# Performance work log

Hardware: AMD Instinct MI355X
Metric: run time of the kernel (lower is better)

## Reference

```python
import jax, jax.numpy as jnp
import numpy as np
from jax import lax

HDIM = 64
KDIM = 256
RATE = 0.999
EPS = 1e-6


def _l2norm(v, axis=-1):
    # matches F.normalize(dim=1) with default eps=1e-12
    n = jnp.sqrt(jnp.sum(v * v, axis=axis, keepdims=True))
    return v / jnp.maximum(n, 1e-12)


def setup_inputs() -> dict:
    key = jax.random.key(0)
    k1, k2 = jax.random.split(key)
    x = jax.random.normal(k1, (4, HDIM, 256, 256), dtype=jnp.float32)
    units = jax.random.normal(k2, (KDIM, HDIM), dtype=jnp.float32)  # nn.Embedding(kdim, hdim)
    return {"x": x, "units": units}


def reference(x, units):
    b, c, h, w = x.shape
    xf = jnp.transpose(x, (0, 2, 3, 1)).reshape(-1, c)        # [n, c]
    xd = lax.stop_gradient(xf)                                 # update uses x.detach()
    m = lax.stop_gradient(units)                               # units.weight.data (no grad)

    xn = _l2norm(xf, axis=1)                                   # [n, c]
    mn = _l2norm(m, axis=1)                                    # [k, c]
    score = jnp.matmul(xn, mn.T)                               # [n, k]
    n = xf.shape[0]

    for _ in range(3):
        # EMA codebook update from hard assignments (scatter-sum via segment_sum)
        idx = jnp.argmax(score, axis=1)                        # [n]
        embed_sum = jax.ops.segment_sum(xd, idx, num_segments=KDIM)          # [k, c]
        counts = jax.ops.segment_sum(jnp.ones((n,), xd.dtype), idx, num_segments=KDIM)  # [k]
        embed_mean = embed_sum / (counts + EPS)[:, None]       # [k, c]
        m = m * RATE + embed_mean * (1.0 - RATE)
        mn = _l2norm(m, axis=1)
        score = jnp.matmul(xn, mn.T)

    soft_label = jax.nn.softmax(score, axis=1)                 # [n, k]
    out = jnp.matmul(soft_label, m)                            # [n, c]
    out = out.reshape(b, h, w, c).transpose(0, 3, 1, 2)        # [b, c, h, w]
    return out
```

## Files before the change

kernel.cpp:

```cpp
#include <hip/hip_runtime.h>
#include <math.h>

#define HW 65536
#define NROW 262144
#define KK 256
#define R3_F 0.997002999f
#define E3_F 0.002997001f
#define NPART 1024

typedef __attribute__((ext_vector_type(8))) short short8;
typedef __attribute__((ext_vector_type(4))) float floatx4;

#define MFMA16(A, B, C) __builtin_amdgcn_mfma_f32_16x16x32_bf16(A, B, C, 0, 0, 0)

union U8 { unsigned u[4]; short8 v; };

__device__ __forceinline__ unsigned short f2bf(float f) {
    unsigned u = __float_as_uint(f);
    u = (u + 0x7FFFu + ((u >> 16) & 1u)) >> 16;
    return (unsigned short)u;
}
__device__ __forceinline__ float bf2f(unsigned hi) {
    return __uint_as_float(hi << 16);
}

__global__ __launch_bounds__(64) void k_init(const float* __restrict__ units,
                                             float* __restrict__ m,
                                             unsigned short* __restrict__ mn) {
    int k = blockIdx.x, c = threadIdx.x;
    float v = units[(k << 6) | c];
    m[(k << 6) | c] = v;
    float ss = v * v;
#pragma unroll
    for (int off = 32; off; off >>= 1) ss += __shfl_xor(ss, off, 64);
    mn[(k << 6) | c] = f2bf(v / fmaxf(sqrtf(ss), 1e-12f));
}

__global__ __launch_bounds__(512, 4) void k_pass1(const float* __restrict__ x,
                                                  const unsigned short* __restrict__ mn,
                                                  unsigned short* __restrict__ psums,
                                                  float* __restrict__ pcnts,
                                                  float* __restrict__ inv_norms,
                                                  unsigned short* __restrict__ xn,
                                                  int write_xn) {
    __shared__ unsigned short xrc[256 * 74];
    __shared__ unsigned short smn[KK * 72];
    __shared__ unsigned int lidx[64];
    __shared__ float lcnt[256];
    __shared__ float sInv[256];
    unsigned int* xrc32 = (unsigned int*)xrc;

    const int tid = threadIdx.x, wave = tid >> 6, lane = tid & 63;
    const int quad = lane >> 4, l15 = lane & 15;
    const int rowbase = blockIdx.x * 256;
    const int b = rowbase >> 16, p0 = rowbase & 65535;
    const float* xb = x + (((size_t)(b * 64)) << 16) + p0;

    if (tid < 256) lcnt[tid] = 0.f;
    for (int i = tid; i < KK * 64; i += 512) smn[(i >> 6) * 72 + (i & 63)] = mn[i];

    {
        int cp = tid >> 4, rq = tid & 15;
        const float* xc0 = xb + (((size_t)(cp * 2)) << 16);
        const float* xc1 = xb + (((size_t)(cp * 2 + 1)) << 16);
#pragma unroll
        for (int i = 0; i < 4; i++) {
            int rg = rq + i * 16;
            float4 v0 = *(const float4*)(xc0 + rg * 4);
            float4 v1 = *(const float4*)(xc1 + rg * 4);
            xrc32[(rg * 4 + 0) * 37 + cp] = (unsigned)f2bf(v0.x) | ((unsigned)f2bf(v1.x) << 16);
            xrc32[(rg * 4 + 1) * 37 + cp] = (unsigned)f2bf(v0.y) | ((unsigned)f2bf(v1.y) << 16);
            xrc32[(rg * 4 + 2) * 37 + cp] = (unsigned)f2bf(v0.z) | ((unsigned)f2bf(v1.z) << 16);
            xrc32[(rg * 4 + 3) * 37 + cp] = (unsigned)f2bf(v0.w) | ((unsigned)f2bf(v1.w) << 16);
        }
    }
    __syncthreads();

    if (tid < 256) {
        float ss = 0.f;
#pragma unroll
        for (int i = 0; i < 32; i++) {
            unsigned u = xrc32[tid * 37 + i];
            float f0 = bf2f(u & 0xffffu), f1 = bf2f(u >> 16);
            ss += f0 * f0 + f1 * f1;
        }
        float invv = 1.0f / fmaxf(sqrtf(ss), 1e-12f);
        sInv[tid] = invv;
        inv_norms[rowbase + tid] = invv;
    }
    __syncthreads();

#pragma unroll
    for (int mt = 0; mt < 2; mt++) {
        int rloc = wave * 32 + mt * 16 + l15;
        U8 a0, a1;
#pragma unroll
        for (int i = 0; i < 4; i++) {
            a0.u[i] = xrc32[rloc * 37 + quad * 4 + i];
            a1.u[i] = xrc32[rloc * 37 + 16 + quad * 4 + i];
        }
        int best[4] = {0, 0, 0, 0};
        for (int nt = 0; nt < 16; nt++) {
            const unsigned short* bp = &smn[(nt * 16 + l15) * 72 + quad * 8];
            short8 b0 = *(const short8*)bp;
            short8 b1 = *(const short8*)(bp + 32);
            floatx4 acc = {0.f, 0.f, 0.f, 0.f};
            acc = MFMA16(a0.v, b0, acc);
            acc = MFMA16(a1.v, b1, acc);
#pragma unroll
            for (int rg = 0; rg < 4; rg++) {
                int pk = (__float_as_int(acc[rg] + 16.0f) & ~255) | (nt * 16 + l15);
                best[rg] = max(best[rg], pk);
            }
        }
#pragma unroll
        for (int off = 1; off <= 8; off <<= 1)
#pragma unroll
            for (int rg = 0; rg < 4; rg++)
                best[rg] = max(best[rg], __shfl_xor(best[rg], off, 64));
        if (l15 == 0) {
            unsigned v = (unsigned)(best[0] & 255) | ((unsigned)(best[1] & 255) << 8)
                       | ((unsigned)(best[2] & 255) << 16) | ((unsigned)(best[3] & 255) << 24);
            lidx[wave * 8 + mt * 4 + quad] = v;
        }
    }

    if (write_xn) {
        unsigned int* xnu = (unsigned int*)xn + (size_t)rowbase * 32;
#pragma unroll
        for (int i = 0; i < 8; i++) {
            int idx2 = i * 512 + tid;
            int row = idx2 >> 4, c2 = idx2 & 15;
            unsigned u0 = xrc32[row * 37 + c2 * 2];
            unsigned u1 = xrc32[row * 37 + c2 * 2 + 1];
            float fv = sInv[row];
            uint2 w;
            w.x = (unsigned)f2bf(bf2f(u0 & 0xffffu) * fv) | ((unsigned)f2bf(bf2f(u0 >> 16) * fv) << 16);
            w.y = (unsigned)f2bf(bf2f(u1 & 0xffffu) * fv) | ((unsigned)f2bf(bf2f(u1 >> 16) * fv) << 16);
            *(uint2*)(xnu + (size_t)idx2 * 2) = w;
        }
    }
    __syncthreads();

    {
        int ch = tid >> 3, rb = tid & 7;
        unsigned short* xT = smn;
        const int cb = ch * 264, rbb = rb * 32;
#pragma unroll
        for (int w = 0; w < 4; w++) {
            int wq = ((w + rb) & 3) * 8;
            short8 t;
#pragma unroll
            for (int j = 0; j < 8; j++)
                t[j] = (short)xrc[(rbb + wq + j) * 74 + ch];
            *(short8*)&xT[cb + rbb + wq] = t;
        }
    }
    __syncthreads();

    {
        const unsigned short* xT = smn;
        int mtg = wave >> 1;
        int ntg = wave & 1;
        floatx4 acc[4][2] = {{{0.f,0.f,0.f,0.f},{0.f,0.f,0.f,0.f}},
                             {{0.f,0.f,0.f,0.f},{0.f,0.f,0.f,0.f}},
                             {{0.f,0.f,0.f,0.f},{0.f,0.f,0.f,0.f}},
                             {{0.f,0.f,0.f,0.f},{0.f,0.f,0.f,0.f}}};
        for (int ks = 0; ks < 8; ks++) {
            unsigned id01 = lidx[ks * 8 + quad * 2 + 0];
            unsigned id23 = lidx[ks * 8 + quad * 2 + 1];
            short8 bf[2];
#pragma unroll
            for (int n = 0; n < 2; n++) {
                int ch = (ntg * 2 + n) * 16 + l15;
                bf[n] = *(const short8*)&xT[ch * 264 + ks * 32 + quad * 8];
            }
#pragma unroll
            for (int mtl = 0; mtl < 4; mtl++) {
                unsigned cl = (unsigned)((mtg * 4 + mtl) * 16 + l15);
                U8 a;
#pragma unroll
                for (int d = 0; d < 4; d++) {
                    unsigned src = (d < 2) ? id01 : id23;
                    unsigned blo = (src >> ((d & 1) * 16)) & 255u;
                    unsigned bhi = (src >> ((d & 1) * 16 + 8)) & 255u;
                    a.u[d] = (blo == cl ? 0x3F80u : 0u) | (bhi == cl ? 0x3F800000u : 0u);
                }
#pragma unroll
                for (int n = 0; n < 2; n++)
                    acc[mtl][n] = MFMA16(a.v, bf[n], acc[mtl][n]);
            }
        }
        unsigned short* ps = psums + (size_t)blockIdx.x * 16384;
#pragma unroll
        for (int mtl = 0; mtl < 4; mtl++) {
            int cl0 = (mtg * 4 + mtl) * 16 + quad * 4;
#pragma unroll
            for (int n = 0; n < 2; n++) {
                int ch = (ntg * 2 + n) * 16 + l15;
#pragma unroll
                for (int rg = 0; rg < 4; rg++)
                    ps[(cl0 + rg) * 64 + ch] = f2bf(acc[mtl][n][rg]);
            }
        }
    }
    if (tid < 256) {
        unsigned myb = (lidx[tid >> 2] >> ((tid & 3) * 8)) & 255u;
        atomicAdd(&lcnt[myb], 1.0f);
    }
    __syncthreads();
    if (tid < 256) pcnts[blockIdx.x * 256 + tid] = lcnt[tid];
}

__global__ __launch_bounds__(1024) void k_update3(float* __restrict__ m,
                                                  unsigned short* __restrict__ mn,
                                                  const unsigned short* __restrict__ psums,
                                                  const float* __restrict__ pcnts,
                                                  unsigned short* __restrict__ mTg) {
    __shared__ float acc8[128 * 68];
    __shared__ float scnt[1024];
    const int k = blockIdx.x, tid = threadIdx.x;
    const uint4* ps4 = (const uint4*)psums;
    const int col = tid & 7, g = tid >> 3;

    float s[8] = {0.f,0.f,0.f,0.f,0.f,0.f,0.f,0.f};
#pragma unroll
    for (int i = 0; i < 8; i++) {
        int pb = g + i * 128;
        uint4 v = ps4[(size_t)pb * 2048 + k * 8 + col];
        s[0] += bf2f(v.x & 0xffffu); s[1] += bf2f(v.x >> 16);
        s[2] += bf2f(v.y & 0xffffu); s[3] += bf2f(v.y >> 16);
        s[4] += bf2f(v.z & 0xffffu); s[5] += bf2f(v.z >> 16);
        s[6] += bf2f(v.w & 0xffffu); s[7] += bf2f(v.w >> 16);
    }
#pragma unroll
    for (int j = 0; j < 8; j++) acc8[g * 68 + col * 8 + j] = s[j];
    scnt[tid] = pcnts[tid * 256 + k];
    __syncthreads();

    if (tid < 64) {
        float tot = 0.f;
        for (int g2 = 0; g2 < 128; g2++) tot += acc8[g2 * 68 + tid];
        float cnt = 0.f;
#pragma unroll
        for (int q = 0; q < 16; q++) cnt += scnt[tid + 64 * q];
#pragma unroll
        for (int off = 32; off; off >>= 1) cnt += __shfl_xor(cnt, off, 64);
        float mean = tot / (cnt + 1e-6f);
        float v = m[(k << 6) | tid] * R3_F + mean * E3_F;
        m[(k << 6) | tid] = v;
        mTg[tid * 256 + k] = f2bf(v);
        float ss = v * v;
#pragma unroll
        for (int off = 32; off; off >>= 1) ss += __shfl_xor(ss, off, 64);
        mn[(k << 6) | tid] = f2bf(v / fmaxf(sqrtf(ss), 1e-12f));
    }
}

__global__ __launch_bounds__(512, 4) void k_final_fast(const unsigned short* __restrict__ xn,
                                                       const unsigned short* __restrict__ mn,
                                                       const unsigned short* __restrict__ mTg,
                                                       float* __restrict__ out) {
    __shared__ unsigned short smn[KK * 64];
    __shared__ unsigned short smT[64 * KK];

    const int tid = threadIdx.x;
    for (int i = tid; i < 2048; i += 512) {
        int row = i >> 3, c = i & 7;
        *(short8*)&smn[row * 64 + ((c ^ (row & 7)) << 3)] = *(const short8*)(mn + i * 8);
    }
    for (int j = tid; j < 2048; j += 512) {
        int ch = j >> 5, cp = j & 31;
        *(short8*)&smT[ch * 256 + ((cp ^ (ch & 7)) << 3)] = *(const short8*)(mTg + j * 8);
    }
    __syncthreads();

    const int wave = tid >> 6, lane = tid & 63;
    const int quad = lane >> 4, l15 = lane & 15;
    const int s7 = l15 & 7;
    const bool hi2 = (quad & 2) != 0, odd = (quad & 1) != 0;

    const int r0 = (blockIdx.x * 8 + wave) * 16;
    const int r = r0 + l15;
    const int b = r0 >> 16, p0 = r0 & 65535;

    short8 a0 = *(const short8*)(xn + (size_t)r * 64 + quad * 8);
    short8 a1 = *(const short8*)(xn + (size_t)r * 64 + 32 + quad * 8);

    float ls = 0.f;
    floatx4 oacc[4] = {{0.f,0.f,0.f,0.f},{0.f,0.f,0.f,0.f},{0.f,0.f,0.f,0.f},{0.f,0.f,0.f,0.f}};

    for (int kt2 = 0; kt2 < 8; kt2++) {
        unsigned W[2][2];
#pragma unroll
        for (int h = 0; h < 2; h++) {
            int kt = kt2 * 2 + h;
            const unsigned short* bp = &smn[(kt * 16 + l15) * 64];
            short8 b0 = *(const short8*)(bp + ((quad ^ s7) << 3));
            short8 b1 = *(const short8*)(bp + (((4 + quad) ^ s7) << 3));
            floatx4 acc = {0.f, 0.f, 0.f, 0.f};
            acc = MFMA16(b0, a0, acc);
            acc = MFMA16(b1, a1, acc);
            float e0 = __expf(acc[0]), e1 = __expf(acc[1]);
            float e2 = __expf(acc[2]), e3 = __expf(acc[3]);
            ls += (e0 + e1) + (e2 + e3);
            W[h][0] = (unsigned)f2bf(e0) | ((unsigned)f2bf(e1) << 16);
            W[h][1] = (unsigned)f2bf(e2) | ((unsigned)f2bf(e3) << 16);
        }
        unsigned memA[2], memB[2];
#pragma unroll
        for (int p = 0; p < 2; p++) {
            unsigned send = hi2 ? W[0][p] : W[1][p];
            unsigned recv = (unsigned)__shfl_xor((int)send, 32, 64);
            unsigned keep = hi2 ? W[1][p] : W[0][p];
            memA[p] = hi2 ? recv : keep;
            memB[p] = hi2 ? keep : recv;
        }
        U8 ap;
#pragma unroll
        for (int p = 0; p < 2; p++) {
            unsigned send2 = odd ? memA[p] : memB[p];
            unsigned recv2 = (unsigned)__shfl_xor((int)send2, 16, 64);
            ap.u[p]     = odd ? recv2 : memA[p];
            ap.u[2 + p] = odd ? memB[p] : recv2;
        }
#pragma unroll
        for (int nt = 0; nt < 4; nt++) {
            short8 bm = *(const short8*)&smT[(nt * 16 + l15) * 256 + (((kt2 * 4 + quad) ^ s7) << 3)];
            oacc[nt] = MFMA16(ap.v, bm, oacc[nt]);
        }
    }

    ls += __shfl_xor(ls, 16, 64);
    ls += __shfl_xor(ls, 32, 64);
    float il = 1.0f / ls;
    float il4[4];
#pragma unroll
    for (int rg = 0; rg < 4; rg++) il4[rg] = __shfl(il, quad * 4 + rg, 64);

#pragma unroll
    for (int nt = 0; nt < 4; nt++) {
        floatx4 w;
#pragma unroll
        for (int rg = 0; rg < 4; rg++) w[rg] = oacc[nt][rg] * il4[rg];
        float* op = out + (((size_t)(b * 64 + nt * 16 + l15)) << 16) + p0 + quad * 4;
        *(floatx4*)op = w;
    }
}

__global__ __launch_bounds__(512, 4) void k_final_legacy(const float* __restrict__ x,
                                                         const unsigned short* __restrict__ mn,
                                                         const float* __restrict__ m,
                                                         const float* __restrict__ inv_norms,
                                                         float* __restrict__ out) {
    __shared__ unsigned short smn[KK * 72];
    __shared__ unsigned short smT[64 * 264];
    __shared__ unsigned short sP[8 * 640];

    const int tid = threadIdx.x;
    for (int i = tid; i < KK * 64; i += 512) smn[(i >> 6) * 72 + (i & 63)] = mn[i];
    for (int i = tid; i < KK * 64; i += 512) smT[(i & 63) * 264 + (i >> 6)] = f2bf(m[i]);
    __syncthreads();

    const int wave = tid >> 6, lane = tid & 63;
    const int quad = lane >> 4, l15 = lane & 15;

    const int r0 = (blockIdx.x * 8 + wave) * 16;
    const int r = r0 + l15;
    const int b = r0 >> 16, p0 = r0 & 65535;
    const float* xp = x + (((size_t)(b * 64)) << 16) + (p0 + l15);

    float xv[16];
#pragma unroll
    for (int j = 0; j < 8; j++) {
        xv[j]     = xp[((size_t)(quad * 8 + j)) << 16];
        xv[8 + j] = xp[((size_t)(32 + quad * 8 + j)) << 16];
    }
    const float inv = inv_norms[r];
    short8 a0, a1;
#pragma unroll
    for (int j = 0; j < 8; j++) {
        a0[j] = (short)f2bf(xv[j] * inv);
        a1[j] = (short)f2bf(xv[8 + j] * inv);
    }

    unsigned short* Pw = sP + wave * 640;
    float ls[4] = {0.f, 0.f, 0.f, 0.f};
    floatx4 oacc[4] = {{0.f,0.f,0.f,0.f},{0.f,0.f,0.f,0.f},{0.f,0.f,0.f,0.f},{0.f,0.f,0.f,0.f}};

    for (int kt2 = 0; kt2 < 8; kt2++) {
#pragma unroll
        for (int h = 0; h < 2; h++) {
            int kt = kt2 * 2 + h;
            const unsigned short* bp = &smn[(kt * 16 + l15) * 72 + quad * 8];
            short8 b0 = *(const short8*)bp;
            short8 b1 = *(const short8*)(bp + 32);
            floatx4 acc = {0.f, 0.f, 0.f, 0.f};
            acc = MFMA16(a0, b0, acc);
            acc = MFMA16(a1, b1, acc);
#pragma unroll
            for (int rg = 0; rg < 4; rg++) {
                float e = __expf(acc[rg]);
                ls[rg] += e;
                Pw[(quad * 4 + rg) * 40 + h * 16 + l15] = f2bf(e);
            }
        }
        __threadfence_block();
        short8 ap = *(const short8*)&Pw[l15 * 40 + quad * 8];
#pragma unroll
        for (int nt = 0; nt < 4; nt++) {
            short8 bm = *(const short8*)&smT[(nt * 16 + l15) * 264 + kt2 * 32 + quad * 8];
            oacc[nt] = MFMA16(ap, bm, oacc[nt]);
        }
    }

#pragma unroll
    for (int off = 1; off <= 8; off <<= 1)
#pragma unroll
        for (int rg = 0; rg < 4; rg++) ls[rg] += __shfl_xor(ls[rg], off, 64);

    float il[4];
#pragma unroll
    for (int rg = 0; rg < 4; rg++) il[rg] = 1.0f / ls[rg];

#pragma unroll
    for (int nt = 0; nt < 4; nt++) {
        floatx4 w;
#pragma unroll
        for (int rg = 0; rg < 4; rg++) w[rg] = oacc[nt][rg] * il[rg];
        float* op = out + (((size_t)(b * 64 + nt * 16 + l15)) << 16) + p0 + quad * 4;
        *(floatx4*)op = w;
    }
}

extern "C" void kernel_launch(void* const* d_in, const int* in_sizes, int n_in,
                              void* d_out, int out_size, void* d_ws, size_t ws_size,
                              hipStream_t stream) {
    (void)in_sizes; (void)n_in; (void)out_size;
    const float* x     = (const float*)d_in[0];
    const float* units = (const float*)d_in[1];
    float* out = (float*)d_out;

    float* W = (float*)d_ws;
    float* m     = W;
    float* inv   = W + 16384;
    float* pcnts = W + 16384 + NROW;
    unsigned short* psums = (unsigned short*)(pcnts + NPART * 256);
    unsigned short* mn = psums + (size_t)NPART * 16384;
    unsigned short* mT = mn + 16384;
    unsigned short* xn = mT + 16384;

    size_t need_fast = (size_t)(16384 + NROW + NPART * 256) * 4
                     + ((size_t)NPART * 16384 + 32768) * 2
                     + (size_t)NROW * 64 * 2;
    int fast = (ws_size >= need_fast) ? 1 : 0;

    k_init<<<KK, 64, 0, stream>>>(units, m, mn);
    k_pass1<<<NPART, 512, 0, stream>>>(x, mn, psums, pcnts, inv, xn, fast);
    k_update3<<<KK, 1024, 0, stream>>>(m, mn, psums, pcnts, mT);
    if (fast) k_final_fast<<<2048, 512, 0, stream>>>(xn, mn, mT, out);
    else      k_final_legacy<<<2048, 512, 0, stream>>>(x, mn, m, inv, out);
}
```

Before: 176.1 us.

## Use nontemporal loads/stores and read codebook directly from global instead of LDS

Streaming global traffic now goes through nontemporal load and store builtins: the xn writes and reads, the partial sums, counts, inverse norms and final output. The normalized codebook is no longer staged in shared memory in pass1 or the final kernel. The MFMA B operands are read straight from global and rely on cache. Pass1 splits the row-norm reduction over all 512 threads, reuses a separate xT buffer and drops one barrier. Together these cut LDS staging, shrink shared memory and keep streamed data from polluting cache, at the cost of repeated global/L1 reads of the codebook in inner loops.

```diff
diff --git a/kernel.cpp b/kernel.cpp
--- a/kernel.cpp
+++ b/kernel.cpp
@@ -10,6 +10,8 @@
 
 typedef __attribute__((ext_vector_type(8))) short short8;
 typedef __attribute__((ext_vector_type(4))) float floatx4;
+typedef __attribute__((ext_vector_type(2))) unsigned int uint2v;
+typedef __attribute__((ext_vector_type(4))) unsigned int uint4v;
 
 #define MFMA16(A, B, C) __builtin_amdgcn_mfma_f32_16x16x32_bf16(A, B, C, 0, 0, 0)
 
@@ -23,6 +25,10 @@
 __device__ __forceinline__ float bf2f(unsigned hi) {
     return __uint_as_float(hi << 16);
 }
+template <typename T>
+__device__ __forceinline__ void nts(T v, T* p) { __builtin_nontemporal_store(v, p); }
+template <typename T>
+__device__ __forceinline__ T ntl(const T* p) { return __builtin_nontemporal_load(p); }
 
 __global__ __launch_bounds__(64) void k_init(const float* __restrict__ units,
                                              float* __restrict__ m,
@@ -44,7 +50,7 @@
                                                   unsigned short* __restrict__ xn,
                                                   int write_xn) {
     __shared__ unsigned short xrc[256 * 74];
-    __shared__ unsigned short smn[KK * 72];
+    __shared__ unsigned short xT[64 * 264];
     __shared__ unsigned int lidx[64];
     __shared__ float lcnt[256];
     __shared__ float sInv[256];
@@ -57,7 +63,6 @@
     const float* xb = x + (((size_t)(b * 64)) << 16) + p0;
 
     if (tid < 256) lcnt[tid] = 0.f;
-    for (int i = tid; i < KK * 64; i += 512) smn[(i >> 6) * 72 + (i & 63)] = mn[i];
 
     {
         int cp = tid >> 4, rq = tid & 15;
@@ -76,17 +81,21 @@
     }
     __syncthreads();
 
-    if (tid < 256) {
+    {
+        int row = tid >> 1, half = tid & 1;
         float ss = 0.f;
 #pragma unroll
-        for (int i = 0; i < 32; i++) {
-            unsigned u = xrc32[tid * 37 + i];
+        for (int i = 0; i < 16; i++) {
+            unsigned u = xrc32[row * 37 + half * 16 + i];
             float f0 = bf2f(u & 0xffffu), f1 = bf2f(u >> 16);
             ss += f0 * f0 + f1 * f1;
         }
-        float invv = 1.0f / fmaxf(sqrtf(ss), 1e-12f);
-        sInv[tid] = invv;
-        inv_norms[rowbase + tid] = invv;
+        ss += __shfl_xor(ss, 1, 64);
+        if (half == 0) {
+            float invv = 1.0f / fmaxf(sqrtf(ss), 1e-12f);
+            sInv[row] = invv;
+            nts(invv, &inv_norms[rowbase + row]);
+        }
     }
     __syncthreads();
 
@@ -101,7 +110,7 @@
         }
         int best[4] = {0, 0, 0, 0};
         for (int nt = 0; nt < 16; nt++) {
-            const unsigned short* bp = &smn[(nt * 16 + l15) * 72 + quad * 8];
+            const unsigned short* bp = mn + (nt * 16 + l15) * 64 + quad * 8;
             short8 b0 = *(const short8*)bp;
             short8 b1 = *(const short8*)(bp + 32);
             floatx4 acc = {0.f, 0.f, 0.f, 0.f};
@@ -134,17 +143,15 @@
             unsigned u0 = xrc32[row * 37 + c2 * 2];
             unsigned u1 = xrc32[row * 37 + c2 * 2 + 1];
             float fv = sInv[row];
-            uint2 w;
+            uint2v w;
             w.x = (unsigned)f2bf(bf2f(u0 & 0xffffu) * fv) | ((unsigned)f2bf(bf2f(u0 >> 16) * fv) << 16);
             w.y = (unsigned)f2bf(bf2f(u1 & 0xffffu) * fv) | ((unsigned)f2bf(bf2f(u1 >> 16) * fv) << 16);
-            *(uint2*)(xnu + (size_t)idx2 * 2) = w;
-        }
-    }
-    __syncthreads();
+            nts(w, (uint2v*)(xnu + (size_t)idx2 * 2));
+        }
+    }
 
     {
         int ch = tid >> 3, rb = tid & 7;
-        unsigned short* xT = smn;
         const int cb = ch * 264, rbb = rb * 32;
 #pragma unroll
         for (int w = 0; w < 4; w++) {
@@ -159,7 +166,6 @@
     __syncthreads();
 
     {
-        const unsigned short* xT = smn;
         int mtg = wave >> 1;
         int ntg = wave & 1;
         floatx4 acc[4][2] = {{{0.f,0.f,0.f,0.f},{0.f,0.f,0.f,0.f}},
@@ -200,7 +206,7 @@
                 int ch = (ntg * 2 + n) * 16 + l15;
 #pragma unroll
                 for (int rg = 0; rg < 4; rg++)
-                    ps[(cl0 + rg) * 64 + ch] = f2bf(acc[mtl][n][rg]);
+                    nts(f2bf(acc[mtl][n][rg]), &ps[(cl0 + rg) * 64 + ch]);
             }
         }
     }
@@ -209,7 +215,7 @@
         atomicAdd(&lcnt[myb], 1.0f);
     }
     __syncthreads();
-    if (tid < 256) pcnts[blockIdx.x * 256 + tid] = lcnt[tid];
+    if (tid < 256) nts(lcnt[tid], &pcnts[blockIdx.x * 256 + tid]);
 }
 
 __global__ __launch_bounds__(1024) void k_update3(float* __restrict__ m,
@@ -220,14 +226,14 @@
     __shared__ float acc8[128 * 68];
     __shared__ float scnt[1024];
     const int k = blockIdx.x, tid = threadIdx.x;
-    const uint4* ps4 = (const uint4*)psums;
+    const uint4v* ps4 = (const uint4v*)psums;
     const int col = tid & 7, g = tid >> 3;
 
     float s[8] = {0.f,0.f,0.f,0.f,0.f,0.f,0.f,0.f};
 #pragma unroll
     for (int i = 0; i < 8; i++) {
         int pb = g + i * 128;
-        uint4 v = ps4[(size_t)pb * 2048 + k * 8 + col];
+        uint4v v = ntl(&ps4[(size_t)pb * 2048 + k * 8 + col]);
         s[0] += bf2f(v.x & 0xffffu); s[1] += bf2f(v.x >> 16);
         s[2] += bf2f(v.y & 0xffffu); s[3] += bf2f(v.y >> 16);
         s[4] += bf2f(v.z & 0xffffu); s[5] += bf2f(v.z >> 16);
@@ -261,14 +267,9 @@
                                                        const unsigned short* __restrict__ mn,
                                                        const unsigned short* __restrict__ mTg,
                                                        float* __restrict__ out) {
-    __shared__ unsigned short smn[KK * 64];
     __shared__ unsigned short smT[64 * KK];
 
     const int tid = threadIdx.x;
-    for (int i = tid; i < 2048; i += 512) {
-        int row = i >> 3, c = i & 7;
-        *(short8*)&smn[row * 64 + ((c ^ (row & 7)) << 3)] = *(const short8*)(mn + i * 8);
-    }
     for (int j = tid; j < 2048; j += 512) {
         int ch = j >> 5, cp = j & 31;
         *(short8*)&smT[ch * 256 + ((cp ^ (ch & 7)) << 3)] = *(const short8*)(mTg + j * 8);
@@ -284,8 +285,8 @@
     const int r = r0 + l15;
     const int b = r0 >> 16, p0 = r0 & 65535;
 
-    short8 a0 = *(const short8*)(xn + (size_t)r * 64 + quad * 8);
-    short8 a1 = *(const short8*)(xn + (size_t)r * 64 + 32 + quad * 8);
+    short8 a0 = ntl((const short8*)(xn + (size_t)r * 64 + quad * 8));
+    short8 a1 = ntl((const short8*)(xn + (size_t)r * 64 + 32 + quad * 8));
 
     float ls = 0.f;
     floatx4 oacc[4] = {{0.f,0.f,0.f,0.f},{0.f,0.f,0.f,0.f},{0.f,0.f,0.f,0.f},{0.f,0.f,0.f,0.f}};
@@ -295,9 +296,9 @@
 #pragma unroll
         for (int h = 0; h < 2; h++) {
             int kt = kt2 * 2 + h;
-            const unsigned short* bp = &smn[(kt * 16 + l15) * 64];
-            short8 b0 = *(const short8*)(bp + ((quad ^ s7) << 3));
-            short8 b1 = *(const short8*)(bp + (((4 + quad) ^ s7) << 3));
+            const unsigned short* bp = mn + (kt * 16 + l15) * 64 + quad * 8;
+            short8 b0 = *(const short8*)bp;
+            short8 b1 = *(const short8*)(bp + 32);
             floatx4 acc = {0.f, 0.f, 0.f, 0.f};
             acc = MFMA16(b0, a0, acc);
             acc = MFMA16(b1, a1, acc);
@@ -344,7 +345,7 @@
 #pragma unroll
         for (int rg = 0; rg < 4; rg++) w[rg] = oacc[nt][rg] * il4[rg];
         float* op = out + (((size_t)(b * 64 + nt * 16 + l15)) << 16) + p0 + quad * 4;
-        *(floatx4*)op = w;
+        nts(w, (floatx4*)op);
     }
 }
 
```

New measurement: 247.7 us. 1.41x slower.
